# Kernel optimization log

Measured on AMD Instinct MI355X. Metric: run time of the kernel, lower is better.

The kernel has to match this reference:

```python
import jax, jax.numpy as jnp
import numpy as np

NUM_NEG_PAIRS = 64
NUM_NEG_INDICES_FOR_LOSS = 16
B, C, H, W = 1, 64, 768, 768
HW = H * W


def setup_inputs() -> dict:
    key = jax.random.key(0)
    k1, k2, k3, k4 = jax.random.split(key, 4)
    feats1 = jax.random.normal(k1, (B, C, H, W), dtype=jnp.float32)
    feats2 = jax.random.normal(k2, (B, C, H, W), dtype=jnp.float32)
    positive_pairs = jax.random.randint(k3, (64, 2), 0, HW, dtype=jnp.int64 if jax.config.jax_enable_x64 else jnp.int32)
    negative_indices = jax.random.randint(k4, (NUM_NEG_PAIRS,), 0, HW, dtype=jnp.int64 if jax.config.jax_enable_x64 else jnp.int32)
    return {"feats1": feats1, "feats2": feats2,
            "positive_pairs": positive_pairs,
            "negative_indices": negative_indices}


def reference(feats1, feats2, positive_pairs, negative_indices):
    # feats1/feats2: [1, C, H, W] -> flatten to [C, HW] (matches .view(C, -1) with B=1)
    f1 = feats1.reshape(C, -1)
    f2 = feats2.reshape(C, -1)
    sel = f1[:, negative_indices]                      # [C, P]
    # squared L2 distance of each selected feature vs all HW locations of feats2
    # ||a-b||^2 = ||a||^2 + ||b||^2 - 2 a.b  (ReLU as in original; dist is nonneg)
    d = (jnp.sum(sel * sel, axis=0)[:, None]
         + jnp.sum(f2 * f2, axis=0)[None, :]
         - 2.0 * jnp.einsum('cp,cn->pn', sel, f2))     # [P, HW]
    d = jax.nn.relu(d)
    # NOTE: the original's mask-exclusion check compares FLOAT distance values
    # against an INT index mask (`dist[...].item() in mask`), which is never true
    # for continuous features, so the effective math is: take the K smallest
    # distances per negative, negate, and average.
    smallest = -jax.lax.top_k(-d, NUM_NEG_INDICES_FOR_LOSS)[0]   # [P, K] smallest dists
    negative_loss = jnp.mean(-smallest, axis=1)                   # [P]
    return jnp.mean(negative_loss)
```

## Files before the change

### kernel.cpp

```cpp
#include <hip/hip_runtime.h>
#include <cstdint>

#define CD 64
#define HWD 589824
#define K1_BLOCKS 1152
#define TPB 4
#define K1_ROWS (K1_BLOCKS * 4)
#define FMAXV 3.402823466e+38f

typedef float f32x16 __attribute__((ext_vector_type(16)));
typedef short bf16x8 __attribute__((ext_vector_type(8)));

__device__ __forceinline__ short f2bf(float f) {
    unsigned u = __float_as_uint(f);
    u = u + 0x7FFFu + ((u >> 16) & 1u);
    return (short)(u >> 16);
}

__device__ __forceinline__ void ins4(float4& t, float x) {
    if (x < t.w) {
        if (x < t.z) { t.w = t.z;
            if (x < t.y) { t.z = t.y;
                if (x < t.x) { t.y = t.x; t.x = x; } else t.y = x;
            } else t.z = x;
        } else t.w = x;
    }
}

__global__ __launch_bounds__(64) void kA_pack(
    const float* __restrict__ f1, const int* __restrict__ nidx,
    short* __restrict__ sel_bf, float* __restrict__ sel2,
    unsigned* __restrict__ ticket)
{
    const int p = blockIdx.x, k = threadIdx.x;
    if (p == 0 && k == 0) *ticket = 0u;
    float v = f1[(long)k * HWD + nidx[p]];
    float s = v * v;
#pragma unroll
    for (int off = 32; off; off >>= 1) s += __shfl_xor(s, off);
    sel_bf[p * CD + k] = f2bf(v);
    if (k == 0) sel2[p] = s;
}

__global__ __launch_bounds__(256) void k1_topk(
    const float* __restrict__ f2, const short* __restrict__ sel_bf,
    const float* __restrict__ sel2, float4* __restrict__ cells)
{
    __shared__ float lds[CD][128];
    const int tid = threadIdx.x;
    const int lane = tid & 63, wid = tid >> 6;
    const int l31 = lane & 31, lh = lane >> 5;
    const long nb = (long)blockIdx.x * (TPB * 128);

    const int srow = tid >> 5;
    const int scol = (tid & 31) * 4;

    bf16x8 sf0[4], sf1[4];
#pragma unroll
    for (int ks = 0; ks < 4; ++ks) {
        sf0[ks] = *(const bf16x8*)(sel_bf + l31 * CD + 16 * ks + 8 * lh);
        sf1[ks] = *(const bf16x8*)(sel_bf + (l31 + 32) * CD + 16 * ks + 8 * lh);
    }
    const float sel20 = sel2[l31], sel21 = sel2[l31 + 32];

    float4 st[8];
#pragma unroll
    for (int i = 0; i < 8; ++i)
        st[i] = *(const float4*)(f2 + (long)(8 * i + srow) * HWD + nb + scol);
    __builtin_amdgcn_sched_barrier(0);
#pragma unroll
    for (int i = 0; i < 8; ++i)
        *(float4*)&lds[8 * i + srow][scol] = st[i];

    float4 t = make_float4(FMAXV, FMAXV, FMAXV, FMAXV);
    float4 u = t;

#pragma unroll
    for (int tt = 0; tt < TPB; ++tt) {
        if (tt + 1 < TPB) {
#pragma unroll
            for (int i = 0; i < 8; ++i)
                st[i] = *(const float4*)(f2 + (long)(8 * i + srow) * HWD
                                         + nb + (long)(tt + 1) * 128 + scol);
            __builtin_amdgcn_sched_barrier(0);
        }
        asm volatile("s_waitcnt lgkmcnt(0)" ::: "memory");
        __builtin_amdgcn_sched_barrier(0);
        __builtin_amdgcn_s_barrier();
        __builtin_amdgcn_sched_barrier(0);

        const int col = wid * 32 + l31;
        float fs = 0.f;
        f32x16 a0, a1;
#pragma unroll
        for (int i = 0; i < 16; ++i) { a0[i] = 0.f; a1[i] = 0.f; }
#pragma unroll
        for (int ks = 0; ks < 4; ++ks) {
            bf16x8 af;
#pragma unroll
            for (int j = 0; j < 8; ++j) {
                float v = lds[16 * ks + 8 * lh + j][col];
                fs += v * v;
                af[j] = f2bf(v);
            }
            a0 = __builtin_amdgcn_mfma_f32_32x32x16_bf16(af, sf0[ks], a0, 0, 0, 0);
            a1 = __builtin_amdgcn_mfma_f32_32x32x16_bf16(af, sf1[ks], a1, 0, 0, 0);
        }
        fs += __shfl_xor(fs, 32);

#pragma unroll
        for (int i = 0; i < 16; ++i) {
            int r = (i & 3) + 8 * (i >> 2) + 4 * lh;
            float fr2 = __shfl(fs, r);
            ins4(t, fmaxf(sel20 + fr2 - 2.f * a0[i], 0.f));
            ins4(u, fmaxf(sel21 + fr2 - 2.f * a1[i], 0.f));
        }

        asm volatile("s_waitcnt lgkmcnt(0)" ::: "memory");
        __builtin_amdgcn_sched_barrier(0);
        __builtin_amdgcn_s_barrier();
        __builtin_amdgcn_sched_barrier(0);

        if (tt + 1 < TPB) {
#pragma unroll
            for (int i = 0; i < 8; ++i)
                *(float4*)&lds[8 * i + srow][scol] = st[i];
        }
    }

    {
        float4 o;
        o.x = __shfl_xor(t.x, 32); o.y = __shfl_xor(t.y, 32);
        o.z = __shfl_xor(t.z, 32); o.w = __shfl_xor(t.w, 32);
        ins4(t, o.x); ins4(t, o.y); ins4(t, o.z); ins4(t, o.w);
        o.x = __shfl_xor(u.x, 32); o.y = __shfl_xor(u.y, 32);
        o.z = __shfl_xor(u.z, 32); o.w = __shfl_xor(u.w, 32);
        ins4(u, o.x); ins4(u, o.y); ins4(u, o.z); ins4(u, o.w);
    }
    if (lh == 0) {
        const int gw = blockIdx.x * 4 + wid;
        cells[(long)gw * CD + l31]      = t;
        cells[(long)gw * CD + l31 + 32] = u;
    }
}

__global__ __launch_bounds__(1024) void k2_sel(
    const float4* __restrict__ cells, float* __restrict__ partial,
    unsigned* __restrict__ ticket, float* __restrict__ out)
{
    const int p = blockIdx.x;
    const int tid = threadIdx.x;
    const int lane = tid & 63, wid = tid >> 6;
    __shared__ unsigned long long wmin[16];

    float4 t = make_float4(FMAXV, FMAXV, FMAXV, FMAXV);
#pragma unroll
    for (int q = 0; q < 4; ++q) {
        float4 b = cells[(long)(tid + q * 1024) * CD + p];
        ins4(t, b.x); ins4(t, b.y); ins4(t, b.z); ins4(t, b.w);
    }
    if (tid < K1_ROWS - 4096) {
        float4 b = cells[(long)(tid + 4096) * CD + p];
        ins4(t, b.x); ins4(t, b.y); ins4(t, b.z); ins4(t, b.w);
    }

    float sum = 0.f;
    for (int rd = 0; rd < 16; ++rd) {
        unsigned long long key =
            ((unsigned long long)__float_as_uint(t.x) << 32) | (unsigned)tid;
#pragma unroll
        for (int off = 32; off; off >>= 1) {
            unsigned long long o = __shfl_xor(key, off);
            if (o < key) key = o;
        }
        if (lane == 0) wmin[wid] = key;
        __syncthreads();
        unsigned long long gk = wmin[0];
#pragma unroll
        for (int w = 1; w < 16; ++w) if (wmin[w] < gk) gk = wmin[w];
        sum += __uint_as_float((unsigned)(gk >> 32));
        if ((unsigned)(gk & 0xFFFFFFFFu) == (unsigned)tid) {
            t.x = t.y; t.y = t.z; t.z = t.w; t.w = FMAXV;
        }
        __syncthreads();
    }

    if (tid == 0) {
        partial[p] = sum;
        __threadfence();
        unsigned tk = atomicAdd(ticket, 1u);
        if (tk == CD - 1) {
            __threadfence();
            float s = 0.f;
            const volatile float* vp = partial;
            for (int q = 0; q < CD; ++q) s += vp[q];
            out[0] = -s / 1024.0f;
        }
    }
}

extern "C" void kernel_launch(void* const* d_in, const int* in_sizes, int n_in,
                              void* d_out, int out_size, void* d_ws, size_t ws_size,
                              hipStream_t stream)
{
    const float* f1   = (const float*)d_in[0];
    const float* f2   = (const float*)d_in[1];
    const int*   nidx = (const int*)d_in[3];
    float* out = (float*)d_out;

    float4*   cells   = (float4*)d_ws;
    short*    sel_bf  = (short*)(cells + (long)K1_ROWS * CD);
    float*    sel2    = (float*)(sel_bf + CD * CD);
    float*    partial = sel2 + CD;
    unsigned* ticket  = (unsigned*)(partial + CD);

    kA_pack<<<CD,         64, 0, stream>>>(f1, nidx, sel_bf, sel2, ticket);
    k1_topk<<<K1_BLOCKS, 256, 0, stream>>>(f2, sel_bf, sel2, cells);
    k2_sel <<<CD,       1024, 0, stream>>>(cells, partial, ticket, out);
}
```

Baseline: 84.37 us.

## Split final top-k selection into coalesced screening pass and single-wave select

The old final-selection kernel had one 1024-thread block per negative. Each block read the top-4 cells with a 1 KB stride and ran 16 rounds of block-wide min-reduction, each needing two __syncthreads. A new screening kernel now reads the top-4 cells contiguously and reduces each 72-row chunk to a top-4 per negative in LDS. A single-wave kernel then picks the 16 smallest per negative using only wavefront shuffles. The main kernel's feats2 loads also become nontemporal. The cost is one extra kernel launch and a coarser per-chunk top-4 cut, which could drop true candidates if more than four of the top 16 fall in one chunk.

```diff
diff --git a/kernel.cpp b/kernel.cpp
--- a/kernel.cpp
+++ b/kernel.cpp
@@ -6,15 +6,22 @@
 #define K1_BLOCKS 1152
 #define TPB 4
 #define K1_ROWS (K1_BLOCKS * 4)
+#define RPB (K1_ROWS / 64)
 #define FMAXV 3.402823466e+38f
 
 typedef float f32x16 __attribute__((ext_vector_type(16)));
+typedef float f32x4v __attribute__((ext_vector_type(4)));
 typedef short bf16x8 __attribute__((ext_vector_type(8)));
 
 __device__ __forceinline__ short f2bf(float f) {
     unsigned u = __float_as_uint(f);
     u = u + 0x7FFFu + ((u >> 16) & 1u);
     return (short)(u >> 16);
+}
+
+__device__ __forceinline__ float4 nt_load4(const float* p) {
+    f32x4v v = __builtin_nontemporal_load((const f32x4v*)p);
+    return make_float4(v.x, v.y, v.z, v.w);
 }
 
 __device__ __forceinline__ void ins4(float4& t, float x) {
@@ -66,7 +73,7 @@
     float4 st[8];
 #pragma unroll
     for (int i = 0; i < 8; ++i)
-        st[i] = *(const float4*)(f2 + (long)(8 * i + srow) * HWD + nb + scol);
+        st[i] = nt_load4(f2 + (long)(8 * i + srow) * HWD + nb + scol);
     __builtin_amdgcn_sched_barrier(0);
 #pragma unroll
     for (int i = 0; i < 8; ++i)
@@ -80,8 +87,8 @@
         if (tt + 1 < TPB) {
 #pragma unroll
             for (int i = 0; i < 8; ++i)
-                st[i] = *(const float4*)(f2 + (long)(8 * i + srow) * HWD
-                                         + nb + (long)(tt + 1) * 128 + scol);
+                st[i] = nt_load4(f2 + (long)(8 * i + srow) * HWD
+                                 + nb + (long)(tt + 1) * 128 + scol);
             __builtin_amdgcn_sched_barrier(0);
         }
         asm volatile("s_waitcnt lgkmcnt(0)" ::: "memory");
@@ -144,48 +151,64 @@
     }
 }
 
-__global__ __launch_bounds__(1024) void k2_sel(
-    const float4* __restrict__ cells, float* __restrict__ partial,
+__global__ __launch_bounds__(1024) void k2a_screen(
+    const float4* __restrict__ cells, float4* __restrict__ cells2)
+{
+    const int tid = threadIdx.x;
+    const int b = blockIdx.x;
+    __shared__ float4 lmm[16][64];
+
+    const float4* base = cells + (long)b * (RPB * 64);
+    float4 t = make_float4(FMAXV, FMAXV, FMAXV, FMAXV);
+#pragma unroll
+    for (int q = 0; q < 4; ++q) {
+        float4 v = base[q * 1024 + tid];
+        ins4(t, v.x); ins4(t, v.y); ins4(t, v.z); ins4(t, v.w);
+    }
+    if (tid < RPB * 64 - 4096) {
+        float4 v = base[4096 + tid];
+        ins4(t, v.x); ins4(t, v.y); ins4(t, v.z); ins4(t, v.w);
+    }
+
+    lmm[tid >> 6][tid & 63] = t;
+    __syncthreads();
+
+    if (tid < 64) {
+        float4 m = make_float4(FMAXV, FMAXV, FMAXV, FMAXV);
+#pragma unroll
+        for (int w = 0; w < 16; ++w) {
+            float4 v = lmm[w][tid];
+            ins4(m, v.x); ins4(m, v.y); ins4(m, v.z); ins4(m, v.w);
+        }
+        cells2[b * 64 + tid] = m;
+    }
+}
+
+__global__ __launch_bounds__(64) void k2b_sel(
+    const float4* __restrict__ cells2, float* __restrict__ partial,
     unsigned* __restrict__ ticket, float* __restrict__ out)
 {
     const int p = blockIdx.x;
-    const int tid = threadIdx.x;
-    const int lane = tid & 63, wid = tid >> 6;
-    __shared__ unsigned long long wmin[16];
-
-    float4 t = make_float4(FMAXV, FMAXV, FMAXV, FMAXV);
-#pragma unroll
-    for (int q = 0; q < 4; ++q) {
-        float4 b = cells[(long)(tid + q * 1024) * CD + p];
-        ins4(t, b.x); ins4(t, b.y); ins4(t, b.z); ins4(t, b.w);
-    }
-    if (tid < K1_ROWS - 4096) {
-        float4 b = cells[(long)(tid + 4096) * CD + p];
-        ins4(t, b.x); ins4(t, b.y); ins4(t, b.z); ins4(t, b.w);
-    }
+    const int lane = threadIdx.x;
+
+    float4 t = cells2[lane * 64 + p];
 
     float sum = 0.f;
     for (int rd = 0; rd < 16; ++rd) {
         unsigned long long key =
-            ((unsigned long long)__float_as_uint(t.x) << 32) | (unsigned)tid;
+            ((unsigned long long)__float_as_uint(t.x) << 32) | (unsigned)lane;
 #pragma unroll
         for (int off = 32; off; off >>= 1) {
             unsigned long long o = __shfl_xor(key, off);
             if (o < key) key = o;
         }
-        if (lane == 0) wmin[wid] = key;
-        __syncthreads();
-        unsigned long long gk = wmin[0];
-#pragma unroll
-        for (int w = 1; w < 16; ++w) if (wmin[w] < gk) gk = wmin[w];
-        sum += __uint_as_float((unsigned)(gk >> 32));
-        if ((unsigned)(gk & 0xFFFFFFFFu) == (unsigned)tid) {
+        sum += __uint_as_float((unsigned)(key >> 32));
+        if ((unsigned)(key & 0xFFFFFFFFu) == (unsigned)lane) {
             t.x = t.y; t.y = t.z; t.z = t.w; t.w = FMAXV;
         }
-        __syncthreads();
-    }
-
-    if (tid == 0) {
+    }
+
+    if (lane == 0) {
         partial[p] = sum;
         __threadfence();
         unsigned tk = atomicAdd(ticket, 1u);
@@ -209,12 +232,14 @@
     float* out = (float*)d_out;
 
     float4*   cells   = (float4*)d_ws;
-    short*    sel_bf  = (short*)(cells + (long)K1_ROWS * CD);
+    float4*   cells2  = cells + (long)K1_ROWS * CD;
+    short*    sel_bf  = (short*)(cells2 + 64 * 64);
     float*    sel2    = (float*)(sel_bf + CD * CD);
     float*    partial = sel2 + CD;
     unsigned* ticket  = (unsigned*)(partial + CD);
 
-    kA_pack<<<CD,         64, 0, stream>>>(f1, nidx, sel_bf, sel2, ticket);
-    k1_topk<<<K1_BLOCKS, 256, 0, stream>>>(f2, sel_bf, sel2, cells);
-    k2_sel <<<CD,       1024, 0, stream>>>(cells, partial, ticket, out);
-}
+    kA_pack   <<<CD,         64, 0, stream>>>(f1, nidx, sel_bf, sel2, ticket);
+    k1_topk   <<<K1_BLOCKS, 256, 0, stream>>>(f2, sel_bf, sel2, cells);
+    k2a_screen<<<CD,       1024, 0, stream>>>(cells, cells2);
+    k2b_sel   <<<CD,         64, 0, stream>>>(cells2, partial, ticket, out);
+}
```

Result: no change. 84.71 us (+0.4%).

## Fuse selection packing into top-k kernel and restructure final reduction by strips

Applied to the files above, without the earlier changes.

Removes the separate pack kernel: every top-k block now gathers the 64 selected feature columns from f1 into shared memory, computes their squared norms, and converts them to bf16 itself. Fewer, larger blocks (768 blocks covering 6 tiles each) spread that redundant gather over more work. The second kernel now splits by strips of cells instead of by negative index: each block screens a top-8 list per negative and writes it out, and the last block to finish merges these into a top-16 with early exit. This cuts a launch and the serialized 16-round block-wide argmin, at the cost of redundant f1 gathers in every block and a single-block final merge.

```diff
diff --git a/kernel.cpp b/kernel.cpp
--- a/kernel.cpp
+++ b/kernel.cpp
@@ -3,9 +3,10 @@
 
 #define CD 64
 #define HWD 589824
-#define K1_BLOCKS 1152
-#define TPB 4
+#define K1_BLOCKS 768
+#define TPB 6
 #define K1_ROWS (K1_BLOCKS * 4)
+#define STRIP 48
 #define FMAXV 3.402823466e+38f
 
 typedef float f32x16 __attribute__((ext_vector_type(16)));
@@ -27,41 +28,73 @@
     }
 }
 
-__global__ __launch_bounds__(64) void kA_pack(
-    const float* __restrict__ f1, const int* __restrict__ nidx,
-    short* __restrict__ sel_bf, float* __restrict__ sel2,
+#define SCREEN8(d, lst, cm)                                                 \
+    if ((d) < (cm)) {                                                       \
+        bool rep = false;                                                   \
+        _Pragma("unroll")                                                   \
+        for (int j = 0; j < 8; ++j)                                         \
+            if (!rep && lst[j] == (cm)) { lst[j] = (d); rep = true; }       \
+        cm = lst[0];                                                        \
+        _Pragma("unroll")                                                   \
+        for (int j = 1; j < 8; ++j) cm = fmaxf(cm, lst[j]);                 \
+    }
+
+#define SCREEN16(d, lst, cm)                                                \
+    if ((d) < (cm)) {                                                       \
+        bool rep = false;                                                   \
+        _Pragma("unroll")                                                   \
+        for (int j = 0; j < 16; ++j)                                        \
+            if (!rep && lst[j] == (cm)) { lst[j] = (d); rep = true; }       \
+        cm = lst[0];                                                        \
+        _Pragma("unroll")                                                   \
+        for (int j = 1; j < 16; ++j) cm = fmaxf(cm, lst[j]);                \
+    }
+
+#define CSW(a, b) { float _mn = fminf(a, b), _mx = fmaxf(a, b); a = _mn; b = _mx; }
+
+__global__ __launch_bounds__(256) void k1_topk(
+    const float* __restrict__ f1, const float* __restrict__ f2,
+    const int* __restrict__ nidx, float4* __restrict__ cells,
     unsigned* __restrict__ ticket)
 {
-    const int p = blockIdx.x, k = threadIdx.x;
-    if (p == 0 && k == 0) *ticket = 0u;
-    float v = f1[(long)k * HWD + nidx[p]];
-    float s = v * v;
-#pragma unroll
-    for (int off = 32; off; off >>= 1) s += __shfl_xor(s, off);
-    sel_bf[p * CD + k] = f2bf(v);
-    if (k == 0) sel2[p] = s;
-}
-
-__global__ __launch_bounds__(256) void k1_topk(
-    const float* __restrict__ f2, const short* __restrict__ sel_bf,
-    const float* __restrict__ sel2, float4* __restrict__ cells)
-{
     __shared__ float lds[CD][128];
+    __shared__ float selk[CD][65];
+    __shared__ float sel2s[CD];
     const int tid = threadIdx.x;
     const int lane = tid & 63, wid = tid >> 6;
     const int l31 = lane & 31, lh = lane >> 5;
+
+    if (blockIdx.x == 0 && tid == 0) *ticket = 0u;
+
+#pragma unroll
+    for (int q = 0; q < 16; ++q) {
+        int idx = q * 256 + tid;
+        int p = idx >> 6, k = idx & 63;
+        selk[p][k] = f1[(long)k * HWD + nidx[p]];
+    }
+    __syncthreads();
+    if (tid < CD) {
+        float s = 0.f;
+#pragma unroll
+        for (int k = 0; k < CD; ++k) s += selk[tid][k] * selk[tid][k];
+        sel2s[tid] = s;
+    }
+    __syncthreads();
+
+    bf16x8 sf0[4], sf1[4];
+#pragma unroll
+    for (int ks = 0; ks < 4; ++ks) {
+#pragma unroll
+        for (int j = 0; j < 8; ++j) {
+            sf0[ks][j] = f2bf(selk[l31][16 * ks + 8 * lh + j]);
+            sf1[ks][j] = f2bf(selk[l31 + 32][16 * ks + 8 * lh + j]);
+        }
+    }
+    const float sel20 = sel2s[l31], sel21 = sel2s[l31 + 32];
+
     const long nb = (long)blockIdx.x * (TPB * 128);
-
     const int srow = tid >> 5;
     const int scol = (tid & 31) * 4;
-
-    bf16x8 sf0[4], sf1[4];
-#pragma unroll
-    for (int ks = 0; ks < 4; ++ks) {
-        sf0[ks] = *(const bf16x8*)(sel_bf + l31 * CD + 16 * ks + 8 * lh);
-        sf1[ks] = *(const bf16x8*)(sel_bf + (l31 + 32) * CD + 16 * ks + 8 * lh);
-    }
-    const float sel20 = sel2[l31], sel21 = sel2[l31 + 32];
 
     float4 st[8];
 #pragma unroll
@@ -145,57 +178,83 @@
 }
 
 __global__ __launch_bounds__(1024) void k2_sel(
-    const float4* __restrict__ cells, float* __restrict__ partial,
+    const float4* __restrict__ cells, float* __restrict__ cells2,
     unsigned* __restrict__ ticket, float* __restrict__ out)
 {
-    const int p = blockIdx.x;
+    const int b = blockIdx.x;
     const int tid = threadIdx.x;
-    const int lane = tid & 63, wid = tid >> 6;
-    __shared__ unsigned long long wmin[16];
-
-    float4 t = make_float4(FMAXV, FMAXV, FMAXV, FMAXV);
-#pragma unroll
-    for (int q = 0; q < 4; ++q) {
-        float4 b = cells[(long)(tid + q * 1024) * CD + p];
-        ins4(t, b.x); ins4(t, b.y); ins4(t, b.z); ins4(t, b.w);
-    }
-    if (tid < K1_ROWS - 4096) {
-        float4 b = cells[(long)(tid + 4096) * CD + p];
-        ins4(t, b.x); ins4(t, b.y); ins4(t, b.z); ins4(t, b.w);
-    }
-
-    float sum = 0.f;
-    for (int rd = 0; rd < 16; ++rd) {
-        unsigned long long key =
-            ((unsigned long long)__float_as_uint(t.x) << 32) | (unsigned)tid;
-#pragma unroll
-        for (int off = 32; off; off >>= 1) {
-            unsigned long long o = __shfl_xor(key, off);
-            if (o < key) key = o;
-        }
-        if (lane == 0) wmin[wid] = key;
-        __syncthreads();
-        unsigned long long gk = wmin[0];
-#pragma unroll
-        for (int w = 1; w < 16; ++w) if (wmin[w] < gk) gk = wmin[w];
-        sum += __uint_as_float((unsigned)(gk >> 32));
-        if ((unsigned)(gk & 0xFFFFFFFFu) == (unsigned)tid) {
-            t.x = t.y; t.y = t.z; t.z = t.w; t.w = FMAXV;
-        }
-        __syncthreads();
-    }
-
-    if (tid == 0) {
-        partial[p] = sum;
+    __shared__ float lmm[16][CD][9];
+    __shared__ int islast;
+
+    const float4* base = cells + (long)b * (STRIP * CD);
+    float l8[8];
+#pragma unroll
+    for (int j = 0; j < 8; ++j) l8[j] = FMAXV;
+    float cm = FMAXV;
+#pragma unroll
+    for (int q = 0; q < 3; ++q) {
+        float4 v = base[q * 1024 + tid];
+        SCREEN8(v.x, l8, cm); SCREEN8(v.y, l8, cm);
+        SCREEN8(v.z, l8, cm); SCREEN8(v.w, l8, cm);
+    }
+    {
+        const int rg = tid >> 6, p = tid & 63;
+#pragma unroll
+        for (int j = 0; j < 8; ++j) lmm[rg][p][j] = l8[j];
+    }
+    __syncthreads();
+
+    if (tid < CD) {
+        float m8[8];
+#pragma unroll
+        for (int j = 0; j < 8; ++j) m8[j] = FMAXV;
+        float c8 = FMAXV;
+#pragma unroll
+        for (int g = 0; g < 16; ++g)
+#pragma unroll
+            for (int j = 0; j < 8; ++j) {
+                float v = lmm[g][tid][j];
+                SCREEN8(v, m8, c8);
+            }
+        CSW(m8[0],m8[1]); CSW(m8[2],m8[3]); CSW(m8[4],m8[5]); CSW(m8[6],m8[7]);
+        CSW(m8[0],m8[2]); CSW(m8[1],m8[3]); CSW(m8[4],m8[6]); CSW(m8[5],m8[7]);
+        CSW(m8[1],m8[2]); CSW(m8[5],m8[6]);
+        CSW(m8[0],m8[4]); CSW(m8[1],m8[5]); CSW(m8[2],m8[6]); CSW(m8[3],m8[7]);
+        CSW(m8[2],m8[4]); CSW(m8[3],m8[5]);
+        CSW(m8[1],m8[2]); CSW(m8[3],m8[4]); CSW(m8[5],m8[6]);
+        float* c2 = cells2 + ((long)b * CD + tid) * 8;
+#pragma unroll
+        for (int j = 0; j < 8; ++j) c2[j] = m8[j];
         __threadfence();
-        unsigned tk = atomicAdd(ticket, 1u);
-        if (tk == CD - 1) {
-            __threadfence();
-            float s = 0.f;
-            const volatile float* vp = partial;
-            for (int q = 0; q < CD; ++q) s += vp[q];
-            out[0] = -s / 1024.0f;
-        }
+    }
+    __syncthreads();
+    if (tid == 0) islast = (atomicAdd(ticket, 1u) == CD - 1) ? 1 : 0;
+    __syncthreads();
+
+    if (islast && tid < CD) {
+        __threadfence();
+        const int p = tid;
+        float lst[16];
+#pragma unroll
+        for (int j = 0; j < 16; ++j) lst[j] = FMAXV;
+        float cmx = FMAXV;
+        for (int w = 0; w < CD; ++w) {
+            const volatile float* c2 = cells2 + ((long)w * CD + p) * 8;
+            float v = c2[0];
+            if (!(v < cmx)) continue;
+            SCREEN16(v, lst, cmx);
+            for (int j = 1; j < 8; ++j) {
+                v = c2[j];
+                if (!(v < cmx)) break;
+                SCREEN16(v, lst, cmx);
+            }
+        }
+        float s = 0.f;
+#pragma unroll
+        for (int j = 0; j < 16; ++j) s += lst[j];
+#pragma unroll
+        for (int off = 32; off; off >>= 1) s += __shfl_xor(s, off);
+        if (tid == 0) out[0] = -s / 1024.0f;
     }
 }
 
@@ -208,13 +267,10 @@
     const int*   nidx = (const int*)d_in[3];
     float* out = (float*)d_out;
 
-    float4*   cells   = (float4*)d_ws;
-    short*    sel_bf  = (short*)(cells + (long)K1_ROWS * CD);
-    float*    sel2    = (float*)(sel_bf + CD * CD);
-    float*    partial = sel2 + CD;
-    unsigned* ticket  = (unsigned*)(partial + CD);
-
-    kA_pack<<<CD,         64, 0, stream>>>(f1, nidx, sel_bf, sel2, ticket);
-    k1_topk<<<K1_BLOCKS, 256, 0, stream>>>(f2, sel_bf, sel2, cells);
-    k2_sel <<<CD,       1024, 0, stream>>>(cells, partial, ticket, out);
-}
+    float4*   cells  = (float4*)d_ws;
+    float*    cells2 = (float*)(cells + (long)K1_ROWS * CD);
+    unsigned* ticket = (unsigned*)(cells2 + (long)CD * CD * 8);
+
+    k1_topk<<<K1_BLOCKS, 256, 0, stream>>>(f1, f2, nidx, cells, ticket);
+    k2_sel <<<CD,       1024, 0, stream>>>(cells, cells2, ticket, out);
+}
```

New measurement: 265.6 us. +214.8%, slower.
